# Kernel tuning notes

Hardware: AMD Instinct MI355X
Metric: run time of the kernel (lower is better)

Reference implementation:

```python
import jax, jax.numpy as jnp
import numpy as np

K_NBR = 128        # PyG radius(max_num_neighbors=128)
NEG_FILL = -1e9    # mask value for max-aggregation over invalid neighbors


def fps(pos, m):
    # Farthest point sampling on pos [N,2] -> [m] int32 indices (start at 0).
    n = pos.shape[0]
    def step(carry, _):
        min_d2, last = carry
        d2 = jnp.sum((pos - pos[last]) ** 2, axis=-1)
        min_d2 = jnp.minimum(min_d2, d2)
        nxt = jnp.argmax(min_d2).astype(jnp.int32)
        return (min_d2, nxt), nxt
    init = (jnp.full((n,), 1e10, pos.dtype), jnp.int32(0))
    _, idxs = jax.lax.scan(step, init, None, length=m - 1)
    return jnp.concatenate([jnp.zeros((1,), jnp.int32), idxs])


def set_abstraction(x, pos, ratio, r, W, b):
    # x [B,N,C], pos [B,N,2]. FPS centers, radius neighbors (<=K), PointNetConv
    # message = Linear(cat[x_j, pos_j - pos_i]) (PyG MLP with one layer and
    # plain_last=True is a bare Linear), then max-aggregate per center.
    B, N, C = x.shape
    m = int(N * ratio)
    idx = jax.vmap(lambda p: fps(p, m))(pos)                         # [B,m]
    ctr = jnp.take_along_axis(pos, idx[..., None], axis=1)           # [B,m,2]
    d2 = jnp.sum((ctr[:, :, None, :] - pos[:, None, :, :]) ** 2, -1)  # [B,m,N]
    k = min(K_NBR, N)
    neg_d2, nbr = jax.lax.top_k(-d2, k)                              # [B,m,k]
    valid = (-neg_d2) <= r * r                                       # in-radius mask
    gather = jax.vmap(lambda a, i: a[i])                             # per-sample fancy index
    x_j = gather(x, nbr)                                             # [B,m,k,C]
    rel = gather(pos, nbr) - ctr[:, :, None, :]                      # [B,m,k,2]
    msg = jnp.concatenate([x_j, rel], axis=-1) @ W + b               # [B,m,k,F]
    msg = jnp.where(valid[..., None], msg, NEG_FILL)
    return jnp.max(msg, axis=2), ctr                                 # [B,m,F], [B,m,2]


def encoder(x, zones_ids, lf_W1, lf_b1, lf_W2, lf_b2, c1_W, c1_b, c2_W, c2_b, c3_W, c3_b):
    lf = jnp.tanh(jnp.tanh(x @ lf_W1 + lf_b1) @ lf_W2 + lf_b2)       # [B,N,64]
    h = jnp.concatenate([lf, zones_ids], axis=-1)                    # [B,N,65]
    h, pos = set_abstraction(h, x, 0.5, 0.5, c1_W, c1_b)             # [B,N/2,64]
    h, pos = set_abstraction(h, pos, 0.25, 1.0, c2_W, c2_b)          # [B,N/8,128]
    g = jnp.concatenate([h, pos], axis=-1) @ c3_W + c3_b             # [B,N/8,1024]
    gf = jnp.max(g, axis=1, keepdims=True)                           # global max pool -> [B,1,1024]
    return lf, gf


def setup_inputs():
    key = jax.random.key(0)
    ks = jax.random.split(key, 12)
    B, N = 4, 4096
    def lin(kw, kb, fi, fo):
        return (jax.random.normal(kw, (fi, fo), jnp.float32) / np.sqrt(fi),
                jax.random.normal(kb, (fo,), jnp.float32) * 0.01)
    x = jax.random.normal(ks[0], (B, N, 2), jnp.float32) * 4.0  # spread so ball(r) holds <128 pts
    zones_ids = jax.random.uniform(ks[1], (B, N, 1), jnp.float32)
    lf_W1, lf_b1 = lin(ks[2], ks[3], 2, 64)
    lf_W2, lf_b2 = lin(ks[4], ks[5], 64, 64)
    c1_W, c1_b = lin(ks[6], ks[7], 67, 64)
    c2_W, c2_b = lin(ks[8], ks[9], 66, 128)
    c3_W, c3_b = lin(ks[10], ks[11], 130, 1024)
    return {"x": x, "zones_ids": zones_ids, "lf_W1": lf_W1, "lf_b1": lf_b1,
            "lf_W2": lf_W2, "lf_b2": lf_b2, "c1_W": c1_W, "c1_b": c1_b,
            "c2_W": c2_W, "c2_b": c2_b, "c3_W": c3_W, "c3_b": c3_b}


def reference(x, zones_ids, lf_W1, lf_b1, lf_W2, lf_b2, c1_W, c1_b, c2_W, c2_b, c3_W, c3_b):
    return encoder(x, zones_ids, lf_W1, lf_b1, lf_W2, lf_b2,
                   c1_W, c1_b, c2_W, c2_b, c3_W, c3_b)
```

## Files before the change

### kernel.cpp

```cpp
#include <hip/hip_runtime.h>


constexpr int BB = 4;
constexpr int NN = 4096;
constexpr int M1 = 2048;
constexpr int M2 = 512;

typedef float v2f __attribute__((ext_vector_type(2)));

__device__ __forceinline__ float d2_exact(float dx, float dy) {
    return __fadd_rn(__fmul_rn(dx, dx), __fmul_rn(dy, dy));
}

template<int CTRL>
__device__ __forceinline__ unsigned long long dpp64z(unsigned long long v) {
    unsigned lo = (unsigned)__builtin_amdgcn_update_dpp(0, (int)(unsigned)v, CTRL, 0xF, 0xF, true);
    unsigned hi = (unsigned)__builtin_amdgcn_update_dpp(0, (int)(unsigned)(v >> 32), CTRL, 0xF, 0xF, true);
    return ((unsigned long long)hi << 32) | (unsigned long long)lo;
}
template<int CTRL>
__device__ __forceinline__ void pairc(unsigned long long& t1, unsigned long long& t2) {
    unsigned long long o1 = dpp64z<CTRL>(t1);
    unsigned long long o2 = dpp64z<CTRL>(t2);
    bool g = o1 > t1;
    unsigned long long m1 = g ? o1 : t1;
    unsigned long long sm = g ? t1 : o1;
    unsigned long long cn = g ? o2 : t2;
    t2 = cn > sm ? cn : sm;
    t1 = m1;
}
__device__ __forceinline__ unsigned long long readlane64(unsigned long long v, int l) {
    unsigned lo = (unsigned)__builtin_amdgcn_readlane((int)(unsigned)v, l);
    unsigned hi = (unsigned)__builtin_amdgcn_readlane((int)(unsigned)(v >> 32), l);
    return ((unsigned long long)hi << 32) | (unsigned long long)lo;
}

__global__ __launch_bounds__(256) void k_lf_y1(
    const float2* __restrict__ x, const float* __restrict__ zones,
    const float* __restrict__ W1, const float* __restrict__ b1,
    const float* __restrict__ W2, const float* __restrict__ b2,
    const float* __restrict__ c1W, const float* __restrict__ c1b,
    float* __restrict__ out_lf, float* __restrict__ y1)
{
    __shared__ float sh[4][64];
    __shared__ float sl[4][64];
    int tid = threadIdx.x;
    int p = tid >> 6, f = tid & 63;
    size_t pt = (size_t)blockIdx.x * 4 + p;
    float2 xv = x[pt];
    float hid = tanhf(xv.x * W1[f] + xv.y * W1[64 + f] + b1[f]);
    sh[p][f] = hid;
    __syncthreads();
    float acc = b2[f];
#pragma unroll
    for (int c = 0; c < 64; ++c) acc += sh[p][c] * W2[c * 64 + f];
    float lf = tanhf(acc);
    sl[p][f] = lf;
    out_lf[pt * 64 + f] = lf;
    __syncthreads();
    float acc2 = c1b[f] + zones[pt] * c1W[64 * 64 + f]
               + xv.x * c1W[65 * 64 + f] + xv.y * c1W[66 * 64 + f];
#pragma unroll
    for (int c = 0; c < 64; ++c) acc2 += sl[p][c] * c1W[c * 64 + f];
    y1[pt * 64 + f] = acc2;
}

template<int M, int PPT>
__device__ __forceinline__ void fps_core(
    const float2* __restrict__ src, const float2* __restrict__ PTSl,
    float2* __restrict__ centl, unsigned long long (&sl)[2][16],
    int tid, int lane, int wv)
{
#pragma clang fp contract(off)
    constexpr int PP2 = PPT / 2;
    v2f px2[PP2], py2[PP2], md2[PP2];
#pragma unroll
    for (int k = 0; k < PP2; ++k) {
        float2 a = src[tid + (2 * k) * 512];
        float2 b = src[tid + (2 * k + 1) * 512];
        px2[k] = (v2f){a.x, b.x};
        py2[k] = (v2f){a.y, b.y};
        md2[k] = (v2f){1e10f, 1e10f};
    }
    float2 c0 = src[0];
    if (tid == 0) centl[0] = c0;

    float c1x = c0.x, c1y = c0.y, c2x = 0.0f, c2y = 0.0f;
    bool two = false;
    int it = 1;
    unsigned rc = 0;
    while (it < M) {
        int par = (int)(rc & 1u); ++rc;
        v2f vcx = (v2f){c1x, c1x}, vcy = (v2f){c1y, c1y};
#pragma unroll
        for (int k = 0; k < PP2; ++k) {
            v2f dx = px2[k] - vcx, dy = py2[k] - vcy;
            v2f d2 = (dx * dx) + (dy * dy);
            md2[k] = __builtin_elementwise_min(md2[k], d2);
        }
        if (two) {
            v2f wcx = (v2f){c2x, c2x}, wcy = (v2f){c2y, c2y};
#pragma unroll
            for (int k = 0; k < PP2; ++k) {
                v2f dx = px2[k] - wcx, dy = py2[k] - wcy;
                v2f d2 = (dx * dx) + (dy * dy);
                md2[k] = __builtin_elementwise_min(md2[k], d2);
            }
        }
        unsigned long long t1 = 0ull, t2 = 0ull;
#pragma unroll
        for (int s = 0; s < PPT; ++s) {
            float mq = (s & 1) ? md2[s >> 1].y : md2[s >> 1].x;
            unsigned long long key =
                ((unsigned long long)__float_as_uint(mq) << 32)
                | (unsigned long long)(0xFFFFFFFFu - (unsigned)(tid + s * 512));
            bool g = key > t1;
            unsigned long long ns = g ? t1 : (key > t2 ? key : t2);
            t1 = g ? key : t1;
            t2 = ns;
        }
        pairc<0x111>(t1, t2); pairc<0x112>(t1, t2); pairc<0x114>(t1, t2);
        pairc<0x118>(t1, t2); pairc<0x142>(t1, t2); pairc<0x143>(t1, t2);
        if (lane == 63) { sl[par][2 * wv] = t1; sl[par][2 * wv + 1] = t2; }
        __syncthreads();
        unsigned long long a1 = sl[par][2 * (lane & 7)];
        unsigned long long a2 = sl[par][2 * (lane & 7) + 1];
        if (lane >= 8) { a1 = 0ull; a2 = 0ull; }
        pairc<0x111>(a1, a2); pairc<0x112>(a1, a2); pairc<0x114>(a1, a2);
        unsigned long long w1 = readlane64(a1, 7);
        unsigned long long r1 = readlane64(a2, 7);
        int jw = (int)(0xFFFFFFFFu - (unsigned)w1);
        int jr = (int)(0xFFFFFFFFu - (unsigned)r1);
        float mdr = __uint_as_float((unsigned)(r1 >> 32));
        float2 wpt = PTSl[jw];
        float2 rpt = PTSl[jr];
        float ddx = rpt.x - wpt.x, ddy = rpt.y - wpt.y;
        float dd = (ddx * ddx) + (ddy * ddy);
        bool dbl = (it + 1 < M) && (dd >= mdr);
        if (tid == 0) { centl[it] = wpt; if (dbl) centl[it + 1] = rpt; }
        c1x = wpt.x; c1y = wpt.y; c2x = rpt.x; c2y = rpt.y;
        two = dbl;
        it += dbl ? 2 : 1;
    }
}

__global__ __launch_bounds__(512, 2) void k_fps_fused(
    const float2* __restrict__ pos, float* __restrict__ p1out,
    float* __restrict__ p2out)
{
    __shared__ float2 PTS[NN];
    __shared__ float2 cent1[M1];
    __shared__ float2 cent2[M2];
    __shared__ unsigned long long sl[2][16];
    int tid = threadIdx.x, lane = tid & 63, wv = tid >> 6;
    const float2* p = pos + (size_t)blockIdx.x * NN;

    for (int i = tid; i < NN; i += 512) PTS[i] = p[i];
    __syncthreads();

    fps_core<M1, NN / 512>(p, PTS, cent1, sl, tid, lane, wv);
    __syncthreads();
    float2* o1 = (float2*)(p1out + (size_t)blockIdx.x * M1 * 2);
    for (int i = tid; i < M1; i += 512) o1[i] = cent1[i];

    fps_core<M2, M1 / 512>(cent1, cent1, cent2, sl, tid, lane, wv);
    __syncthreads();
    float2* o2 = (float2*)(p2out + (size_t)blockIdx.x * M2 * 2);
    for (int i = tid; i < M2; i += 512) o2[i] = cent2[i];
}

__global__ __launch_bounds__(256) void k_sa(
    const float2* __restrict__ candpos, const float* __restrict__ y,
    const float* __restrict__ ctr, const float* __restrict__ W,
    int NP, int F, int relrow, float r2, float* __restrict__ hout)
{
    __shared__ int cnt;
    __shared__ int list[4096];
    int tid = threadIdx.x;
    int b = blockIdx.y;
    size_t crow = (size_t)b * gridDim.x + blockIdx.x;
    if (tid == 0) cnt = 0;
    __syncthreads();
    float cx = ctr[crow * 2], cy = ctr[crow * 2 + 1];
    const float2* cp = candpos + (size_t)b * NP;
    for (int j = tid; j < NP; j += 256) {
        float2 pj = cp[j];
        float d2 = d2_exact(pj.x - cx, pj.y - cy);
        if (d2 <= r2) { int t = atomicAdd(&cnt, 1); list[t] = j; }
    }
    __syncthreads();
    int n = cnt;
    for (int f = tid; f < F; f += 256) {
        float m = -3.0e38f;
        for (int t = 0; t < n; ++t)
            m = fmaxf(m, y[((size_t)b * NP + list[t]) * F + f]);
        float ct = cx * W[(size_t)relrow * F + f] + cy * W[(size_t)(relrow + 1) * F + f];
        hout[crow * F + f] = m - ct;
    }
}

__global__ __launch_bounds__(128) void k_y2(
    const float* __restrict__ h1, const float* __restrict__ p1,
    const float* __restrict__ W, const float* __restrict__ bb,
    float* __restrict__ y2)
{
    __shared__ float sh[64];
    size_t row = blockIdx.x;
    int f = threadIdx.x;
    if (f < 64) sh[f] = h1[row * 64 + f];
    __syncthreads();
    float acc = bb[f] + p1[row * 2] * W[64 * 128 + f]
              + p1[row * 2 + 1] * W[65 * 128 + f];
#pragma unroll
    for (int c = 0; c < 64; ++c) acc += sh[c] * W[c * 128 + f];
    y2[row * 128 + f] = acc;
}

__global__ __launch_bounds__(256) void k_g(
    const float* __restrict__ h2, const float* __restrict__ p2,
    const float* __restrict__ W3, const float* __restrict__ b3,
    float* __restrict__ part)
{
    int f = blockIdx.x * 256 + threadIdx.x;
    int b = blockIdx.z;
    int i0 = blockIdx.y * 8;
    float acc[8];
    float bbv = b3[f];
#pragma unroll
    for (int ii = 0; ii < 8; ++ii) acc[ii] = bbv;
    const float* hrow = h2 + ((size_t)b * M2 + i0) * 128;
    for (int c = 0; c < 128; ++c) {
        float w = W3[(size_t)c * 1024 + f];
#pragma unroll
        for (int ii = 0; ii < 8; ++ii) acc[ii] += hrow[ii * 128 + c] * w;
    }
    float wx = W3[(size_t)128 * 1024 + f];
    float wy = W3[(size_t)129 * 1024 + f];
    const float* prow = p2 + ((size_t)b * M2 + i0) * 2;
    float m = -3.0e38f;
#pragma unroll
    for (int ii = 0; ii < 8; ++ii) {
        float g = acc[ii] + prow[ii * 2] * wx + prow[ii * 2 + 1] * wy;
        m = fmaxf(m, g);
    }
    part[((size_t)b * 64 + blockIdx.y) * 1024 + f] = m;
}

__global__ __launch_bounds__(256) void k_gmax(const float* __restrict__ part,
                                              float* __restrict__ outg)
{
    int f = blockIdx.x * 256 + threadIdx.x;
    int b = f >> 10, fl = f & 1023;
    float m = -3.0e38f;
#pragma unroll 8
    for (int ig = 0; ig < 64; ++ig)
        m = fmaxf(m, part[((size_t)b * 64 + ig) * 1024 + fl]);
    outg[f] = m;
}

extern "C" void kernel_launch(void* const* d_in, const int* in_sizes, int n_in,
                              void* d_out, int out_size, void* d_ws, size_t ws_size,
                              hipStream_t stream)
{
    const float* x    = (const float*)d_in[0];
    const float* zon  = (const float*)d_in[1];
    const float* lfW1 = (const float*)d_in[2];
    const float* lfb1 = (const float*)d_in[3];
    const float* lfW2 = (const float*)d_in[4];
    const float* lfb2 = (const float*)d_in[5];
    const float* c1W  = (const float*)d_in[6];
    const float* c1b  = (const float*)d_in[7];
    const float* c2W  = (const float*)d_in[8];
    const float* c2b  = (const float*)d_in[9];
    const float* c3W  = (const float*)d_in[10];
    const float* c3b  = (const float*)d_in[11];
    float* out = (float*)d_out;

    char* w = (char*)d_ws;
    float* big = (float*)w;                    w += (size_t)BB * NN * 64 * 4;
    float* p1  = (float*)w;                    w += (size_t)BB * M1 * 2 * 4;
    float* h1  = (float*)w;                    w += (size_t)BB * M1 * 64 * 4;
    float* p2  = (float*)w;                    w += (size_t)BB * M2 * 2 * 4;
    float* h2  = (float*)w;                    w += (size_t)BB * M2 * 128 * 4;
    float* y1 = big, * y2 = big, * part = big;

    k_lf_y1<<<BB * NN / 4, 256, 0, stream>>>((const float2*)x, zon, lfW1, lfb1,
                                             lfW2, lfb2, c1W, c1b, out, y1);
    k_fps_fused<<<BB, 512, 0, stream>>>((const float2*)x, p1, p2);
    k_sa<<<dim3(M1, BB), 256, 0, stream>>>((const float2*)x, y1, p1, c1W,
                                           NN, 64, 65, 0.25f, h1);
    k_y2<<<BB * M1, 128, 0, stream>>>(h1, p1, c2W, c2b, y2);
    k_sa<<<dim3(M2, BB), 256, 0, stream>>>((const float2*)p1, y2, p2, c2W,
                                           M1, 128, 64, 1.0f, h2);
    k_g<<<dim3(4, 64, BB), 256, 0, stream>>>(h2, p2, c3W, c3b, part);
    k_gmax<<<16, 256, 0, stream>>>(part, out + (size_t)BB * NN * 64);
}
```

Measured before the change: 1.684 ms.

## Extend FPS to commit up to eight centers per block-wide reduction round

The farthest-point-sampling loop previously committed one or two centers per block-wide argmax round. It now gathers the top-2 candidates from each wave plus a per-wave third-largest bound. It then picks candidates greedily in every thread for as long as the best updated candidate distance exceeds that bound, up to eight per round. This cuts the number of __syncthreads and cross-wave reduction rounds in the sequential FPS. In exchange it adds a third-value DPP reduction, a 16-candidate serial selection loop per thread, and more distance updates per round.

```diff
diff --git a/kernel.cpp b/kernel.cpp
--- a/kernel.cpp
+++ b/kernel.cpp
@@ -13,9 +13,13 @@
 }
 
 template<int CTRL>
+__device__ __forceinline__ unsigned dppz(unsigned v) {
+    return (unsigned)__builtin_amdgcn_update_dpp(0, (int)v, CTRL, 0xF, 0xF, true);
+}
+template<int CTRL>
 __device__ __forceinline__ unsigned long long dpp64z(unsigned long long v) {
-    unsigned lo = (unsigned)__builtin_amdgcn_update_dpp(0, (int)(unsigned)v, CTRL, 0xF, 0xF, true);
-    unsigned hi = (unsigned)__builtin_amdgcn_update_dpp(0, (int)(unsigned)(v >> 32), CTRL, 0xF, 0xF, true);
+    unsigned lo = dppz<CTRL>((unsigned)v);
+    unsigned hi = dppz<CTRL>((unsigned)(v >> 32));
     return ((unsigned long long)hi << 32) | (unsigned long long)lo;
 }
 template<int CTRL>
@@ -29,6 +33,18 @@
     t2 = cn > sm ? cn : sm;
     t1 = m1;
 }
+template<int CTRL>
+__device__ __forceinline__ void tripc(unsigned& v1, unsigned& v2, unsigned& v3) {
+    unsigned o1 = dppz<CTRL>(v1), o2 = dppz<CTRL>(v2), o3 = dppz<CTRL>(v3);
+    unsigned m1 = v1 > o1 ? v1 : o1, n1 = v1 > o1 ? o1 : v1;
+    unsigned m2 = v2 > o2 ? v2 : o2, n2 = v2 > o2 ? o2 : v2;
+    unsigned m3 = v3 > o3 ? v3 : o3;
+    unsigned a = n1 > m2 ? m2 : n1;
+    v2 = n1 > m2 ? n1 : m2;
+    unsigned b = n2 > m3 ? n2 : m3;
+    v3 = a > b ? a : b;
+    v1 = m1;
+}
 __device__ __forceinline__ unsigned long long readlane64(unsigned long long v, int l) {
     unsigned lo = (unsigned)__builtin_amdgcn_readlane((int)(unsigned)v, l);
     unsigned hi = (unsigned)__builtin_amdgcn_readlane((int)(unsigned)(v >> 32), l);
@@ -68,11 +84,12 @@
 template<int M, int PPT>
 __device__ __forceinline__ void fps_core(
     const float2* __restrict__ src, const float2* __restrict__ PTSl,
-    float2* __restrict__ centl, unsigned long long (&sl)[2][16],
-    int tid, int lane, int wv)
+    float2* __restrict__ centl, unsigned long long (&slk)[2][16],
+    unsigned (&slv)[2][8], int tid, int lane, int wv)
 {
 #pragma clang fp contract(off)
     constexpr int PP2 = PPT / 2;
+    constexpr int PEND = 8;
     v2f px2[PP2], py2[PP2], md2[PP2];
 #pragma unroll
     for (int k = 0; k < PP2; ++k) {
@@ -85,62 +102,100 @@
     float2 c0 = src[0];
     if (tid == 0) centl[0] = c0;
 
-    float c1x = c0.x, c1y = c0.y, c2x = 0.0f, c2y = 0.0f;
-    bool two = false;
+    float pendx[PEND], pendy[PEND];
+    pendx[0] = c0.x; pendy[0] = c0.y;
+    int picks = 1;
     int it = 1;
     unsigned rc = 0;
     while (it < M) {
         int par = (int)(rc & 1u); ++rc;
-        v2f vcx = (v2f){c1x, c1x}, vcy = (v2f){c1y, c1y};
-#pragma unroll
-        for (int k = 0; k < PP2; ++k) {
-            v2f dx = px2[k] - vcx, dy = py2[k] - vcy;
-            v2f d2 = (dx * dx) + (dy * dy);
-            md2[k] = __builtin_elementwise_min(md2[k], d2);
-        }
-        if (two) {
-            v2f wcx = (v2f){c2x, c2x}, wcy = (v2f){c2y, c2y};
-#pragma unroll
-            for (int k = 0; k < PP2; ++k) {
-                v2f dx = px2[k] - wcx, dy = py2[k] - wcy;
+#pragma unroll
+        for (int k = 0; k < PEND; ++k) {
+            if (k >= picks) break;
+            v2f vcx = (v2f){pendx[k], pendx[k]};
+            v2f vcy = (v2f){pendy[k], pendy[k]};
+#pragma unroll
+            for (int q = 0; q < PP2; ++q) {
+                v2f dx = px2[q] - vcx, dy = py2[q] - vcy;
                 v2f d2 = (dx * dx) + (dy * dy);
-                md2[k] = __builtin_elementwise_min(md2[k], d2);
+                md2[q] = __builtin_elementwise_min(md2[q], d2);
             }
         }
         unsigned long long t1 = 0ull, t2 = 0ull;
+        unsigned v1 = 0u, v2 = 0u, v3 = 0u;
 #pragma unroll
         for (int s = 0; s < PPT; ++s) {
             float mq = (s & 1) ? md2[s >> 1].y : md2[s >> 1].x;
-            unsigned long long key =
-                ((unsigned long long)__float_as_uint(mq) << 32)
+            unsigned mb = __float_as_uint(mq);
+            unsigned long long key = ((unsigned long long)mb << 32)
                 | (unsigned long long)(0xFFFFFFFFu - (unsigned)(tid + s * 512));
             bool g = key > t1;
             unsigned long long ns = g ? t1 : (key > t2 ? key : t2);
             t1 = g ? key : t1;
             t2 = ns;
+            bool g1 = mb > v1, g2 = mb > v2, g3 = mb > v3;
+            unsigned nv3 = g2 ? v2 : (g3 ? mb : v3);
+            unsigned nv2 = g1 ? v1 : (g2 ? mb : v2);
+            v1 = g1 ? mb : v1; v2 = nv2; v3 = nv3;
         }
         pairc<0x111>(t1, t2); pairc<0x112>(t1, t2); pairc<0x114>(t1, t2);
         pairc<0x118>(t1, t2); pairc<0x142>(t1, t2); pairc<0x143>(t1, t2);
-        if (lane == 63) { sl[par][2 * wv] = t1; sl[par][2 * wv + 1] = t2; }
+        tripc<0x111>(v1, v2, v3); tripc<0x112>(v1, v2, v3); tripc<0x114>(v1, v2, v3);
+        tripc<0x118>(v1, v2, v3); tripc<0x142>(v1, v2, v3); tripc<0x143>(v1, v2, v3);
+        if (lane == 63) {
+            slk[par][2 * wv] = t1; slk[par][2 * wv + 1] = t2;
+            slv[par][wv] = v3;
+        }
         __syncthreads();
-        unsigned long long a1 = sl[par][2 * (lane & 7)];
-        unsigned long long a2 = sl[par][2 * (lane & 7) + 1];
-        if (lane >= 8) { a1 = 0ull; a2 = 0ull; }
-        pairc<0x111>(a1, a2); pairc<0x112>(a1, a2); pairc<0x114>(a1, a2);
-        unsigned long long w1 = readlane64(a1, 7);
-        unsigned long long r1 = readlane64(a2, 7);
-        int jw = (int)(0xFFFFFFFFu - (unsigned)w1);
-        int jr = (int)(0xFFFFFFFFu - (unsigned)r1);
-        float mdr = __uint_as_float((unsigned)(r1 >> 32));
-        float2 wpt = PTSl[jw];
-        float2 rpt = PTSl[jr];
-        float ddx = rpt.x - wpt.x, ddy = rpt.y - wpt.y;
-        float dd = (ddx * ddx) + (ddy * ddy);
-        bool dbl = (it + 1 < M) && (dd >= mdr);
-        if (tid == 0) { centl[it] = wpt; if (dbl) centl[it + 1] = rpt; }
-        c1x = wpt.x; c1y = wpt.y; c2x = rpt.x; c2y = rpt.y;
-        two = dbl;
-        it += dbl ? 2 : 1;
+        float cmd[16], cpx[16], cpy[16];
+        unsigned clo[16];
+        unsigned B = 0u;
+#pragma unroll
+        for (int w = 0; w < 8; ++w) {
+            unsigned long long a = slk[par][2 * w];
+            unsigned long long b = slk[par][2 * w + 1];
+            cmd[2 * w]     = __uint_as_float((unsigned)(a >> 32));
+            clo[2 * w]     = (unsigned)a;
+            cmd[2 * w + 1] = __uint_as_float((unsigned)(b >> 32));
+            clo[2 * w + 1] = (unsigned)b;
+            unsigned tv = slv[par][w];
+            B = tv > B ? tv : B;
+        }
+#pragma unroll
+        for (int i = 0; i < 16; ++i) {
+            float2 pp = PTSl[(int)(0xFFFFFFFFu - clo[i])];
+            cpx[i] = pp.x; cpy[i] = pp.y;
+        }
+        float Bf = __uint_as_float(B);
+        picks = 0;
+        while (true) {
+            float km = cmd[0];
+#pragma unroll
+            for (int i = 1; i < 16; ++i) km = fmaxf(km, cmd[i]);
+            if (picks > 0 && !(km > Bf)) break;
+            unsigned klo = 0u;
+#pragma unroll
+            for (int i = 0; i < 16; ++i)
+                klo = (cmd[i] == km && clo[i] > klo) ? clo[i] : klo;
+            float kx = 0.0f, ky = 0.0f;
+#pragma unroll
+            for (int i = 0; i < 16; ++i) {
+                bool h = clo[i] == klo;
+                kx = h ? cpx[i] : kx;
+                ky = h ? cpy[i] : ky;
+            }
+            if (tid == 0) centl[it] = make_float2(kx, ky);
+            pendx[picks] = kx; pendy[picks] = ky;
+            ++picks; ++it;
+            if (it >= M || picks >= PEND) break;
+#pragma unroll
+            for (int i = 0; i < 16; ++i) {
+                float dx = cpx[i] - kx, dy = cpy[i] - ky;
+                float d2 = (dx * dx) + (dy * dy);
+                float nm = fminf(cmd[i], d2);
+                cmd[i] = (clo[i] == klo) ? -1.0f : nm;
+            }
+        }
     }
 }
 
@@ -151,19 +206,20 @@
     __shared__ float2 PTS[NN];
     __shared__ float2 cent1[M1];
     __shared__ float2 cent2[M2];
-    __shared__ unsigned long long sl[2][16];
+    __shared__ unsigned long long slk[2][16];
+    __shared__ unsigned slv[2][8];
     int tid = threadIdx.x, lane = tid & 63, wv = tid >> 6;
     const float2* p = pos + (size_t)blockIdx.x * NN;
 
     for (int i = tid; i < NN; i += 512) PTS[i] = p[i];
     __syncthreads();
 
-    fps_core<M1, NN / 512>(p, PTS, cent1, sl, tid, lane, wv);
+    fps_core<M1, NN / 512>(p, PTS, cent1, slk, slv, tid, lane, wv);
     __syncthreads();
     float2* o1 = (float2*)(p1out + (size_t)blockIdx.x * M1 * 2);
     for (int i = tid; i < M1; i += 512) o1[i] = cent1[i];
 
-    fps_core<M2, M1 / 512>(cent1, cent1, cent2, sl, tid, lane, wv);
+    fps_core<M2, M1 / 512>(cent1, cent1, cent2, slk, slv, tid, lane, wv);
     __syncthreads();
     float2* o2 = (float2*)(p2out + (size_t)blockIdx.x * M2 * 2);
     for (int i = tid; i < M2; i += 512) o2[i] = cent2[i];
```

Result: slower. 3.355 ms (+99.2%).

## Pick up to four FPS centers per barrier round from per-wave candidate lists

Applied to the files above, without the earlier changes.

The farthest-point-sampling loop now reduces each wave to its top key plus an upper bound on the next-best distance, then greedily picks up to four centers per block-wide barrier. After each pick, the eight wave candidates' distances are updated against the chosen point, and picking continues while the best one still beats the bound. This cuts the number of __syncthreads rounds in the serial FPS loop, replacing the previous scheme that picked at most two. The cost is more scalar work per round and up to four distance passes per round, and the correctness of the bound logic is subtle.

```diff
diff --git a/kernel.cpp b/kernel.cpp
--- a/kernel.cpp
+++ b/kernel.cpp
@@ -13,9 +13,13 @@
 }
 
 template<int CTRL>
+__device__ __forceinline__ unsigned dppz(unsigned v) {
+    return (unsigned)__builtin_amdgcn_update_dpp(0, (int)v, CTRL, 0xF, 0xF, true);
+}
+template<int CTRL>
 __device__ __forceinline__ unsigned long long dpp64z(unsigned long long v) {
-    unsigned lo = (unsigned)__builtin_amdgcn_update_dpp(0, (int)(unsigned)v, CTRL, 0xF, 0xF, true);
-    unsigned hi = (unsigned)__builtin_amdgcn_update_dpp(0, (int)(unsigned)(v >> 32), CTRL, 0xF, 0xF, true);
+    unsigned lo = dppz<CTRL>((unsigned)v);
+    unsigned hi = dppz<CTRL>((unsigned)(v >> 32));
     return ((unsigned long long)hi << 32) | (unsigned long long)lo;
 }
 template<int CTRL>
@@ -29,11 +33,6 @@
     t2 = cn > sm ? cn : sm;
     t1 = m1;
 }
-__device__ __forceinline__ unsigned long long readlane64(unsigned long long v, int l) {
-    unsigned lo = (unsigned)__builtin_amdgcn_readlane((int)(unsigned)v, l);
-    unsigned hi = (unsigned)__builtin_amdgcn_readlane((int)(unsigned)(v >> 32), l);
-    return ((unsigned long long)hi << 32) | (unsigned long long)lo;
-}
 
 __global__ __launch_bounds__(256) void k_lf_y1(
     const float2* __restrict__ x, const float* __restrict__ zones,
@@ -65,11 +64,26 @@
     y1[pt * 64 + f] = acc2;
 }
 
+#define FC_EXTRACT(i) \
+    unsigned long long kk##i = slk[par][i]; \
+    float cmd##i = __uint_as_float((unsigned)(kk##i >> 32)); \
+    unsigned clo##i = (unsigned)kk##i; \
+    float2 pp##i = PTSl[(int)(0xFFFFFFFFu - clo##i)]; \
+    float cpx##i = pp##i.x; float cpy##i = pp##i.y;
+#define FC_KM(i)  km = fmaxf(km, cmd##i);
+#define FC_KLO(i) klo = (cmd##i == km && clo##i > klo) ? clo##i : klo;
+#define FC_KPOS(i) { bool h = clo##i == klo; kx = h ? cpx##i : kx; ky = h ? cpy##i : ky; }
+#define FC_UPD(i) { float dx_ = cpx##i - kx, dy_ = cpy##i - ky; \
+    float dd_ = (dx_ * dx_) + (dy_ * dy_); \
+    float nm_ = fminf(cmd##i, dd_); \
+    cmd##i = (clo##i == klo) ? -1.0f : nm_; }
+#define FC_ALL(OP) OP(0) OP(1) OP(2) OP(3) OP(4) OP(5) OP(6) OP(7)
+
 template<int M, int PPT>
 __device__ __forceinline__ void fps_core(
     const float2* __restrict__ src, const float2* __restrict__ PTSl,
-    float2* __restrict__ centl, unsigned long long (&sl)[2][16],
-    int tid, int lane, int wv)
+    float2* __restrict__ centl, unsigned long long (&slk)[2][8],
+    unsigned (&slv)[2][8], int tid, int lane, int wv)
 {
 #pragma clang fp contract(off)
     constexpr int PP2 = PPT / 2;
@@ -85,34 +99,32 @@
     float2 c0 = src[0];
     if (tid == 0) centl[0] = c0;
 
-    float c1x = c0.x, c1y = c0.y, c2x = 0.0f, c2y = 0.0f;
-    bool two = false;
+    float p0x = c0.x, p0y = c0.y, p1x = 0.f, p1y = 0.f;
+    float p2x = 0.f, p2y = 0.f, p3x = 0.f, p3y = 0.f;
+    int picks = 1;
     int it = 1;
     unsigned rc = 0;
     while (it < M) {
         int par = (int)(rc & 1u); ++rc;
-        v2f vcx = (v2f){c1x, c1x}, vcy = (v2f){c1y, c1y};
-#pragma unroll
-        for (int k = 0; k < PP2; ++k) {
-            v2f dx = px2[k] - vcx, dy = py2[k] - vcy;
-            v2f d2 = (dx * dx) + (dy * dy);
-            md2[k] = __builtin_elementwise_min(md2[k], d2);
-        }
-        if (two) {
-            v2f wcx = (v2f){c2x, c2x}, wcy = (v2f){c2y, c2y};
-#pragma unroll
-            for (int k = 0; k < PP2; ++k) {
-                v2f dx = px2[k] - wcx, dy = py2[k] - wcy;
-                v2f d2 = (dx * dx) + (dy * dy);
-                md2[k] = __builtin_elementwise_min(md2[k], d2);
+#pragma unroll
+        for (int k = 0; k < 4; ++k) {
+            if (k < picks) {
+                float ax = (k == 0) ? p0x : (k == 1) ? p1x : (k == 2) ? p2x : p3x;
+                float ay = (k == 0) ? p0y : (k == 1) ? p1y : (k == 2) ? p2y : p3y;
+                v2f vcx = (v2f){ax, ax}, vcy = (v2f){ay, ay};
+#pragma unroll
+                for (int q = 0; q < PP2; ++q) {
+                    v2f dx = px2[q] - vcx, dy = py2[q] - vcy;
+                    v2f d2 = (dx * dx) + (dy * dy);
+                    md2[q] = __builtin_elementwise_min(md2[q], d2);
+                }
             }
         }
         unsigned long long t1 = 0ull, t2 = 0ull;
 #pragma unroll
         for (int s = 0; s < PPT; ++s) {
             float mq = (s & 1) ? md2[s >> 1].y : md2[s >> 1].x;
-            unsigned long long key =
-                ((unsigned long long)__float_as_uint(mq) << 32)
+            unsigned long long key = ((unsigned long long)__float_as_uint(mq) << 32)
                 | (unsigned long long)(0xFFFFFFFFu - (unsigned)(tid + s * 512));
             bool g = key > t1;
             unsigned long long ns = g ? t1 : (key > t2 ? key : t2);
@@ -121,26 +133,39 @@
         }
         pairc<0x111>(t1, t2); pairc<0x112>(t1, t2); pairc<0x114>(t1, t2);
         pairc<0x118>(t1, t2); pairc<0x142>(t1, t2); pairc<0x143>(t1, t2);
-        if (lane == 63) { sl[par][2 * wv] = t1; sl[par][2 * wv + 1] = t2; }
+        if (lane == 63) {
+            slk[par][wv] = t1;
+            slv[par][wv] = (unsigned)(t2 >> 32);
+        }
         __syncthreads();
-        unsigned long long a1 = sl[par][2 * (lane & 7)];
-        unsigned long long a2 = sl[par][2 * (lane & 7) + 1];
-        if (lane >= 8) { a1 = 0ull; a2 = 0ull; }
-        pairc<0x111>(a1, a2); pairc<0x112>(a1, a2); pairc<0x114>(a1, a2);
-        unsigned long long w1 = readlane64(a1, 7);
-        unsigned long long r1 = readlane64(a2, 7);
-        int jw = (int)(0xFFFFFFFFu - (unsigned)w1);
-        int jr = (int)(0xFFFFFFFFu - (unsigned)r1);
-        float mdr = __uint_as_float((unsigned)(r1 >> 32));
-        float2 wpt = PTSl[jw];
-        float2 rpt = PTSl[jr];
-        float ddx = rpt.x - wpt.x, ddy = rpt.y - wpt.y;
-        float dd = (ddx * ddx) + (ddy * ddy);
-        bool dbl = (it + 1 < M) && (dd >= mdr);
-        if (tid == 0) { centl[it] = wpt; if (dbl) centl[it + 1] = rpt; }
-        c1x = wpt.x; c1y = wpt.y; c2x = rpt.x; c2y = rpt.y;
-        two = dbl;
-        it += dbl ? 2 : 1;
+        unsigned B = slv[par][0];
+        B = slv[par][1] > B ? slv[par][1] : B;
+        B = slv[par][2] > B ? slv[par][2] : B;
+        B = slv[par][3] > B ? slv[par][3] : B;
+        B = slv[par][4] > B ? slv[par][4] : B;
+        B = slv[par][5] > B ? slv[par][5] : B;
+        B = slv[par][6] > B ? slv[par][6] : B;
+        B = slv[par][7] > B ? slv[par][7] : B;
+        FC_ALL(FC_EXTRACT)
+        float Bf = __uint_as_float(B);
+        picks = 0;
+        while (true) {
+            float km = cmd0;
+            FC_KM(1) FC_KM(2) FC_KM(3) FC_KM(4) FC_KM(5) FC_KM(6) FC_KM(7)
+            if (picks > 0 && !(km > Bf)) break;
+            unsigned klo = 0u;
+            FC_ALL(FC_KLO)
+            float kx = 0.0f, ky = 0.0f;
+            FC_ALL(FC_KPOS)
+            if (tid == 0) centl[it] = make_float2(kx, ky);
+            if (picks == 0)      { p0x = kx; p0y = ky; }
+            else if (picks == 1) { p1x = kx; p1y = ky; }
+            else if (picks == 2) { p2x = kx; p2y = ky; }
+            else                 { p3x = kx; p3y = ky; }
+            ++picks; ++it;
+            if (it >= M || picks >= 4) break;
+            FC_ALL(FC_UPD)
+        }
     }
 }
 
@@ -151,19 +176,20 @@
     __shared__ float2 PTS[NN];
     __shared__ float2 cent1[M1];
     __shared__ float2 cent2[M2];
-    __shared__ unsigned long long sl[2][16];
+    __shared__ unsigned long long slk[2][8];
+    __shared__ unsigned slv[2][8];
     int tid = threadIdx.x, lane = tid & 63, wv = tid >> 6;
     const float2* p = pos + (size_t)blockIdx.x * NN;
 
     for (int i = tid; i < NN; i += 512) PTS[i] = p[i];
     __syncthreads();
 
-    fps_core<M1, NN / 512>(p, PTS, cent1, sl, tid, lane, wv);
+    fps_core<M1, NN / 512>(p, PTS, cent1, slk, slv, tid, lane, wv);
     __syncthreads();
     float2* o1 = (float2*)(p1out + (size_t)blockIdx.x * M1 * 2);
     for (int i = tid; i < M1; i += 512) o1[i] = cent1[i];
 
-    fps_core<M2, M1 / 512>(cent1, cent1, cent2, sl, tid, lane, wv);
+    fps_core<M2, M1 / 512>(cent1, cent1, cent2, slk, slv, tid, lane, wv);
     __syncthreads();
     float2* o2 = (float2*)(p2out + (size_t)blockIdx.x * M2 * 2);
     for (int i = tid; i < M2; i += 512) o2[i] = cent2[i];
```

After: 2.672 ms. 58.7% more time.
